# Kernel optimization log

Measured on AMD Instinct MI355X. Metric: run time of the kernel, lower is better.

The kernel has to match this reference:

```python
import jax, jax.numpy as jnp
import numpy as np

V, H, L, B = 32000, 1024, 2, 64
TEMP = 0.8


def setup_inputs() -> dict:
    key = jax.random.key(0)
    ks = jax.random.split(key, 12)
    sV = 1.0 / np.sqrt(V)
    sH = 1.0 / np.sqrt(H)
    return {
        "x": jax.random.normal(ks[0], (B, V), jnp.float32),
        "hidden_states": jax.random.normal(ks[1], (L, B, H), jnp.float32),
        "cell_states": jax.random.normal(ks[2], (L, B, H), jnp.float32),
        # gate order along axis 1: f, i, o, g
        "Wh": jax.random.uniform(ks[3], (L, 4, H, H), jnp.float32, -sH, sH),
        "bh": jax.random.uniform(ks[4], (L, 4, H), jnp.float32, -sH, sH),
        "Wx0": jax.random.uniform(ks[5], (4, H, V), jnp.float32, -sV, sV),
        "bx0": jax.random.uniform(ks[6], (4, H), jnp.float32, -sV, sV),
        "Wx1": jax.random.uniform(ks[7], (4, H, H), jnp.float32, -sH, sH),
        "bx1": jax.random.uniform(ks[8], (4, H), jnp.float32, -sH, sH),
        "Wdec": jax.random.uniform(ks[9], (V, H), jnp.float32, -sH, sH),
        "bdec": jax.random.uniform(ks[10], (V,), jnp.float32, -sH, sH),
    }


def _lstm_cell(inp, h, c, Wx, bx, Whl, bhl):
    # fused gate pre-activations: [B, 4, H]
    z = (jnp.einsum("ghk,bk->bgh", Wx, inp) + bx[None]
         + jnp.einsum("ghk,bk->bgh", Whl, h) + bhl[None])
    f = jax.nn.sigmoid(z[:, 0])
    i = jax.nn.sigmoid(z[:, 1])
    o = jax.nn.sigmoid(z[:, 2])
    g = jnp.tanh(z[:, 3])
    c_new = f * c + i * g
    out = o * jnp.tanh(c_new)
    return out, c_new


def reference(x, hidden_states, cell_states, Wh, bh, Wx0, bx0, Wx1, bx1, Wdec, bdec):
    wx = [(Wx0, bx0), (Wx1, bx1)]
    outputs, cstates = [], []
    inp = x
    for l in range(L):
        out, c_new = _lstm_cell(inp, hidden_states[l], cell_states[l],
                                wx[l][0], wx[l][1], Wh[l], bh[l])
        outputs.append(out)
        cstates.append(c_new)
        inp = out
    logits = outputs[-1] @ Wdec.T + bdec
    logp = jax.nn.log_softmax(logits / TEMP, axis=-1)
    return logp, jnp.stack(outputs), jnp.stack(cstates)
```

## Files before the change

kernel.cpp:

```cpp
#include <hip/hip_runtime.h>
#include <hip/hip_bf16.h>
#include <cstdint>

#define DI __device__ __forceinline__

typedef __attribute__((ext_vector_type(8))) short short8;
typedef __attribute__((ext_vector_type(4))) float f32x4;
typedef __attribute__((ext_vector_type(4))) int int4v;

DI f32x4 mfma16(short8 a, short8 b, f32x4 c) {
  return __builtin_amdgcn_mfma_f32_16x16x32_bf16(a, b, c, 0, 0, 0);
}

DI uint32_t f2bf(float f) {
  uint32_t u = __float_as_uint(f);
  return (u + 0x7fffu + ((u >> 16) & 1u)) >> 16;
}

DI uint32_t pk2(float a, float b) {
  return f2bf(a) | (f2bf(b) << 16);
}

DI short8 cvt8(float4 a, float4 b) {
  int4v t;
  t.x = (int)pk2(a.x, a.y);
  t.y = (int)pk2(a.z, a.w);
  t.z = (int)pk2(b.x, b.y);
  t.w = (int)pk2(b.z, b.w);
  return __builtin_bit_cast(short8, t);
}

__global__ __launch_bounds__(256, 3) void gates_f32(
    const float* __restrict__ x, const float* __restrict__ hs,
    const float* __restrict__ Wx0, const float* __restrict__ Wh,
    float* __restrict__ zpart) {
  const int y = blockIdx.y;
  const float* A;
  const float* W;
  int ldA, K, steps;
  long kbase;
  if (y < 40) {
    A = x; ldA = 32000; W = Wx0; K = 32000; steps = 25;
    kbase = (long)y * 800;
  } else if (y < 44) {
    A = hs; ldA = 1024; W = Wh; K = 1024; steps = 8;
    kbase = (long)(y - 40) * 256;
  } else {
    A = hs + 65536; ldA = 1024; W = Wh + 4194304; K = 1024; steps = 8;
    kbase = (long)(y - 44) * 256;
  }
  const int tid = threadIdx.x;
  const int wv = tid >> 6;
  const int lane = tid & 63;
  const int l15 = lane & 15;
  const int l4 = lane >> 4;
  const int h = blockIdx.x * 64 + wv * 16 + l15;

  const float* arow[4];
#pragma unroll
  for (int m = 0; m < 4; ++m)
    arow[m] = A + (size_t)(m * 16 + l15) * ldA + kbase + l4 * 8;
  const float* wrow[4];
#pragma unroll
  for (int g = 0; g < 4; ++g)
    wrow[g] = W + (size_t)(g * 1024 + h) * K + kbase + l4 * 8;

  f32x4 acc[4][4];
#pragma unroll
  for (int g = 0; g < 4; ++g)
#pragma unroll
    for (int m = 0; m < 4; ++m)
      acc[g][m] = f32x4{0.f, 0.f, 0.f, 0.f};

  for (int s = 0; s < steps; ++s) {
    short8 af[4];
#pragma unroll
    for (int m = 0; m < 4; ++m) {
      const float* ap = arow[m] + (size_t)s * 32;
      float4 a0 = *(const float4*)ap;
      float4 a1 = *(const float4*)(ap + 4);
      af[m] = cvt8(a0, a1);
    }
#pragma unroll
    for (int g = 0; g < 4; ++g) {
      const float* wp = wrow[g] + (size_t)s * 32;
      float4 w0 = *(const float4*)wp;
      float4 w1 = *(const float4*)(wp + 4);
      short8 bfr = cvt8(w0, w1);
#pragma unroll
      for (int m = 0; m < 4; ++m)
        acc[g][m] = mfma16(af[m], bfr, acc[g][m]);
    }
  }

  float* zp = zpart + (size_t)y * 262144 + (size_t)(l4 * 4) * 4096 + h;
#pragma unroll
  for (int g = 0; g < 4; ++g)
#pragma unroll
    for (int m = 0; m < 4; ++m)
#pragma unroll
      for (int r = 0; r < 4; ++r)
        zp[(size_t)(m * 16 + r) * 4096 + g * 1024] = acc[g][m][r];
}

__global__ __launch_bounds__(256) void gates_b16(
    const ushort* __restrict__ A, const float* __restrict__ W,
    float* __restrict__ zbase) {
  const int chunk = blockIdx.y;
  const long kbase = (long)chunk * 64;
  const int tid = threadIdx.x;
  const int wv = tid >> 6;
  const int lane = tid & 63;
  const int l15 = lane & 15;
  const int l4 = lane >> 4;
  const int h = blockIdx.x * 64 + wv * 16 + l15;

  const ushort* arow[4];
#pragma unroll
  for (int m = 0; m < 4; ++m)
    arow[m] = A + (size_t)(m * 16 + l15) * 1024 + kbase + l4 * 8;
  const float* wrow[4];
#pragma unroll
  for (int g = 0; g < 4; ++g)
    wrow[g] = W + (size_t)(g * 1024 + h) * 1024 + kbase + l4 * 8;

  f32x4 acc[4][4];
#pragma unroll
  for (int g = 0; g < 4; ++g)
#pragma unroll
    for (int m = 0; m < 4; ++m)
      acc[g][m] = f32x4{0.f, 0.f, 0.f, 0.f};

#pragma unroll
  for (int s = 0; s < 2; ++s) {
    short8 af[4];
#pragma unroll
    for (int m = 0; m < 4; ++m)
      af[m] = *(const short8*)(arow[m] + (size_t)s * 32);
#pragma unroll
    for (int g = 0; g < 4; ++g) {
      const float* wp = wrow[g] + (size_t)s * 32;
      float4 w0 = *(const float4*)wp;
      float4 w1 = *(const float4*)(wp + 4);
      short8 bfr = cvt8(w0, w1);
#pragma unroll
      for (int m = 0; m < 4; ++m)
        acc[g][m] = mfma16(af[m], bfr, acc[g][m]);
    }
  }

  float* zp = zbase + (size_t)chunk * 262144 + (size_t)(l4 * 4) * 4096 + h;
#pragma unroll
  for (int g = 0; g < 4; ++g)
#pragma unroll
    for (int m = 0; m < 4; ++m)
#pragma unroll
      for (int r = 0; r < 4; ++r)
        zp[(size_t)(m * 16 + r) * 4096 + g * 1024] = acc[g][m][r];
}

__global__ __launch_bounds__(256) void lstm_cell_k(
    const float* __restrict__ zpart, int nslots,
    const float* __restrict__ bx, const float* __restrict__ bhl,
    const float* __restrict__ c_in,
    float* __restrict__ h_out, float* __restrict__ c_out,
    ushort* __restrict__ h_out_b) {
  int idx = blockIdx.x * 256 + threadIdx.x;
  if (idx >= 64 * 1024) return;
  int h = idx & 1023;
  float z0 = bx[h] + bhl[h];
  float z1 = bx[1024 + h] + bhl[1024 + h];
  float z2 = bx[2048 + h] + bhl[2048 + h];
  float z3 = bx[3072 + h] + bhl[3072 + h];
  int b = idx >> 10;
  const float* zp = zpart + (size_t)b * 4096 + h;
  for (int s = 0; s < nslots; ++s) {
    const float* p = zp + (size_t)s * 262144;
    z0 += p[0];
    z1 += p[1024];
    z2 += p[2048];
    z3 += p[3072];
  }
  float f = 1.f / (1.f + expf(-z0));
  float i = 1.f / (1.f + expf(-z1));
  float o = 1.f / (1.f + expf(-z2));
  float g = tanhf(z3);
  float c = f * c_in[idx] + i * g;
  float hv = o * tanhf(c);
  h_out[idx] = hv;
  c_out[idx] = c;
  h_out_b[idx] = (ushort)f2bf(hv);
}

__global__ __launch_bounds__(64) void gemm_dec(
    const ushort* __restrict__ A, const float* __restrict__ W,
    const float* __restrict__ bias, float* __restrict__ logits) {
  const int lane = threadIdx.x;
  const int l15 = lane & 15;
  const int l4 = lane >> 4;
  const int col = blockIdx.x * 16 + l15;

  const ushort* arow[4];
#pragma unroll
  for (int m = 0; m < 4; ++m)
    arow[m] = A + (size_t)(m * 16 + l15) * 1024 + l4 * 8;
  const float* wrow = W + (size_t)col * 1024 + l4 * 8;

  f32x4 acc[4];
#pragma unroll
  for (int m = 0; m < 4; ++m) acc[m] = f32x4{0.f, 0.f, 0.f, 0.f};

  for (int s = 0; s < 32; ++s) {
    short8 af[4];
#pragma unroll
    for (int m = 0; m < 4; ++m)
      af[m] = *(const short8*)(arow[m] + (size_t)s * 32);
    const float* wp = wrow + (size_t)s * 32;
    float4 w0 = *(const float4*)wp;
    float4 w1 = *(const float4*)(wp + 4);
    short8 bfr = cvt8(w0, w1);
#pragma unroll
    for (int m = 0; m < 4; ++m)
      acc[m] = mfma16(af[m], bfr, acc[m]);
  }

  float bv = bias[col];
  float* lp = logits + (size_t)(l4 * 4) * 32000 + col;
#pragma unroll
  for (int m = 0; m < 4; ++m)
#pragma unroll
    for (int r = 0; r < 4; ++r)
      lp[(size_t)(m * 16 + r) * 32000] = acc[m][r] + bv;
}

__global__ __launch_bounds__(256) void softmax_part1(
    const float* __restrict__ logits, float2* __restrict__ ms) {
  const int cx = blockIdx.x;
  const int b = blockIdx.y;
  const int tid = threadIdx.x;
  const int wv = tid >> 6;
  const int lane = tid & 63;
  const float* row = logits + (size_t)b * 32000 + cx * 8000;
  __shared__ float rbuf[4];

  float m = -1e30f;
  for (int i = tid; i < 8000; i += 256) m = fmaxf(m, row[i]);
#pragma unroll
  for (int d = 1; d < 64; d <<= 1) m = fmaxf(m, __shfl_xor(m, d));
  if (lane == 0) rbuf[wv] = m;
  __syncthreads();
  m = fmaxf(fmaxf(rbuf[0], rbuf[1]), fmaxf(rbuf[2], rbuf[3]));
  __syncthreads();

  float sum = 0.f;
  for (int i = tid; i < 8000; i += 256) sum += expf((row[i] - m) * 1.25f);
#pragma unroll
  for (int d = 1; d < 64; d <<= 1) sum += __shfl_xor(sum, d);
  if (lane == 0) rbuf[wv] = sum;
  __syncthreads();
  if (tid == 0) {
    sum = rbuf[0] + rbuf[1] + rbuf[2] + rbuf[3];
    ms[b * 4 + cx] = make_float2(m, sum);
  }
}

__global__ __launch_bounds__(256) void softmax_part2(
    const float* __restrict__ logits, const float2* __restrict__ ms,
    float* __restrict__ logp) {
  const int cx = blockIdx.x;
  const int b = blockIdx.y;
  const int tid = threadIdx.x;

  float2 p0 = ms[b * 4 + 0], p1 = ms[b * 4 + 1];
  float2 p2 = ms[b * 4 + 2], p3 = ms[b * 4 + 3];
  float M = fmaxf(fmaxf(p0.x, p1.x), fmaxf(p2.x, p3.x));
  float S = p0.y * expf((p0.x - M) * 1.25f) + p1.y * expf((p1.x - M) * 1.25f) +
            p2.y * expf((p2.x - M) * 1.25f) + p3.y * expf((p3.x - M) * 1.25f);
  float lse = logf(S);

  const float* row = logits + (size_t)b * 32000 + cx * 4000;
  float* op = logp + (size_t)b * 32000 + cx * 4000;
  for (int i = tid; i < 4000; i += 256)
    op[i] = (row[i] - M) * 1.25f - lse;
}

extern "C" void kernel_launch(void* const* d_in, const int* in_sizes, int n_in,
                              void* d_out, int out_size, void* d_ws, size_t ws_size,
                              hipStream_t stream) {
  const float* x    = (const float*)d_in[0];
  const float* hs   = (const float*)d_in[1];
  const float* cs   = (const float*)d_in[2];
  const float* Wh   = (const float*)d_in[3];
  const float* bh   = (const float*)d_in[4];
  const float* Wx0  = (const float*)d_in[5];
  const float* bx0  = (const float*)d_in[6];
  const float* Wx1  = (const float*)d_in[7];
  const float* bx1  = (const float*)d_in[8];
  const float* Wdec = (const float*)d_in[9];
  const float* bdec = (const float*)d_in[10];

  float* out   = (float*)d_out;
  float* logp  = out;
  float* houts = out + 2048000;
  float* couts = out + 2179072;

  char* ws = (char*)d_ws;
  ushort* outb   = (ushort*)ws;
  float*  logits = (float*)(ws + 262144);
  float2* ms     = (float2*)(ws + 262144 + 8192000);
  float*  zpart  = (float*)(ws + 262144 + 8192000 + 2048);

  gates_f32<<<dim3(16, 48), 256, 0, stream>>>(x, hs, Wx0, Wh, zpart);

  lstm_cell_k<<<256, 256, 0, stream>>>(zpart, 44, bx0, bh, cs,
                                       houts, couts, outb);

  gates_b16<<<dim3(16, 16), 256, 0, stream>>>(
      outb, Wx1, zpart + (size_t)48 * 262144);

  lstm_cell_k<<<256, 256, 0, stream>>>(zpart + (size_t)44 * 262144, 20,
                                       bx1, bh + 4096, cs + 65536,
                                       houts + 65536, couts + 65536,
                                       outb + 65536);

  gemm_dec<<<2000, 64, 0, stream>>>(outb + 65536, Wdec, bdec, logits);

  softmax_part1<<<dim3(4, 64), 256, 0, stream>>>(logits, ms);
  softmax_part2<<<dim3(8, 64), 256, 0, stream>>>(logits, ms, logp);
}
```

Before: 277.2 us.

## Widen per-lane K contiguity to 128-float strips and cut split-K partial count

Each lane now loads 32 contiguous floats (eight float4s) per step instead of 8, so one row fetch covers four MFMA k-slices. The mapping of K to lanes is permuted consistently for A and W, so the dot products are unchanged. The split-K factor drops (gates_f32 48→29 slots, gates_b16 16→8), which means fewer partial sums to write and reduce in the lstm_cell kernels. The cost is higher register pressure (occupancy hint lowered from 3 to 2) and fewer blocks in flight for the big weight stream.

```diff
diff --git a/kernel.cpp b/kernel.cpp
--- a/kernel.cpp
+++ b/kernel.cpp
@@ -30,24 +30,24 @@
   return __builtin_bit_cast(short8, t);
 }
 
-__global__ __launch_bounds__(256, 3) void gates_f32(
+__global__ __launch_bounds__(256, 2) void gates_f32(
     const float* __restrict__ x, const float* __restrict__ hs,
     const float* __restrict__ Wx0, const float* __restrict__ Wh,
     float* __restrict__ zpart) {
   const int y = blockIdx.y;
   const float* A;
   const float* W;
-  int ldA, K, steps;
+  int ldA, K, nss;
   long kbase;
-  if (y < 40) {
-    A = x; ldA = 32000; W = Wx0; K = 32000; steps = 25;
-    kbase = (long)y * 800;
-  } else if (y < 44) {
-    A = hs; ldA = 1024; W = Wh; K = 1024; steps = 8;
-    kbase = (long)(y - 40) * 256;
+  if (y < 25) {
+    A = x; ldA = 32000; W = Wx0; K = 32000; nss = 10;
+    kbase = (long)y * 1280;
+  } else if (y < 27) {
+    A = hs; ldA = 1024; W = Wh; K = 1024; nss = 4;
+    kbase = (long)(y - 25) * 512;
   } else {
-    A = hs + 65536; ldA = 1024; W = Wh + 4194304; K = 1024; steps = 8;
-    kbase = (long)(y - 44) * 256;
+    A = hs + 65536; ldA = 1024; W = Wh + 4194304; K = 1024; nss = 4;
+    kbase = (long)(y - 27) * 512;
   }
   const int tid = threadIdx.x;
   const int wv = tid >> 6;
@@ -59,11 +59,11 @@
   const float* arow[4];
 #pragma unroll
   for (int m = 0; m < 4; ++m)
-    arow[m] = A + (size_t)(m * 16 + l15) * ldA + kbase + l4 * 8;
+    arow[m] = A + (size_t)(m * 16 + l15) * ldA + kbase + l4 * 32;
   const float* wrow[4];
 #pragma unroll
   for (int g = 0; g < 4; ++g)
-    wrow[g] = W + (size_t)(g * 1024 + h) * K + kbase + l4 * 8;
+    wrow[g] = W + (size_t)(g * 1024 + h) * K + kbase + l4 * 32;
 
   f32x4 acc[4][4];
 #pragma unroll
@@ -72,24 +72,30 @@
     for (int m = 0; m < 4; ++m)
       acc[g][m] = f32x4{0.f, 0.f, 0.f, 0.f};
 
-  for (int s = 0; s < steps; ++s) {
-    short8 af[4];
+  for (int ss = 0; ss < nss; ++ss) {
+    short8 af[4][4];
 #pragma unroll
     for (int m = 0; m < 4; ++m) {
-      const float* ap = arow[m] + (size_t)s * 32;
-      float4 a0 = *(const float4*)ap;
-      float4 a1 = *(const float4*)(ap + 4);
-      af[m] = cvt8(a0, a1);
+      const float* ap = arow[m] + (size_t)ss * 128;
+      float4 av[8];
+#pragma unroll
+      for (int t = 0; t < 8; ++t) av[t] = *(const float4*)(ap + t * 4);
+#pragma unroll
+      for (int j = 0; j < 4; ++j) af[m][j] = cvt8(av[2 * j], av[2 * j + 1]);
     }
 #pragma unroll
     for (int g = 0; g < 4; ++g) {
-      const float* wp = wrow[g] + (size_t)s * 32;
-      float4 w0 = *(const float4*)wp;
-      float4 w1 = *(const float4*)(wp + 4);
-      short8 bfr = cvt8(w0, w1);
-#pragma unroll
-      for (int m = 0; m < 4; ++m)
-        acc[g][m] = mfma16(af[m], bfr, acc[g][m]);
+      const float* wp = wrow[g] + (size_t)ss * 128;
+      float4 wvv[8];
+#pragma unroll
+      for (int t = 0; t < 8; ++t) wvv[t] = *(const float4*)(wp + t * 4);
+#pragma unroll
+      for (int j = 0; j < 4; ++j) {
+        short8 bfr = cvt8(wvv[2 * j], wvv[2 * j + 1]);
+#pragma unroll
+        for (int m = 0; m < 4; ++m)
+          acc[g][m] = mfma16(af[m][j], bfr, acc[g][m]);
+      }
     }
   }
 
@@ -107,7 +113,7 @@
     const ushort* __restrict__ A, const float* __restrict__ W,
     float* __restrict__ zbase) {
   const int chunk = blockIdx.y;
-  const long kbase = (long)chunk * 64;
+  const long kbase = (long)chunk * 128;
   const int tid = threadIdx.x;
   const int wv = tid >> 6;
   const int lane = tid & 63;
@@ -115,14 +121,14 @@
   const int l4 = lane >> 4;
   const int h = blockIdx.x * 64 + wv * 16 + l15;
 
-  const ushort* arow[4];
-#pragma unroll
-  for (int m = 0; m < 4; ++m)
-    arow[m] = A + (size_t)(m * 16 + l15) * 1024 + kbase + l4 * 8;
-  const float* wrow[4];
-#pragma unroll
-  for (int g = 0; g < 4; ++g)
-    wrow[g] = W + (size_t)(g * 1024 + h) * 1024 + kbase + l4 * 8;
+  short8 af[4][4];
+#pragma unroll
+  for (int m = 0; m < 4; ++m) {
+    const ushort* ap = A + (size_t)(m * 16 + l15) * 1024 + kbase + l4 * 32;
+#pragma unroll
+    for (int j = 0; j < 4; ++j)
+      af[m][j] = *(const short8*)(ap + j * 8);
+  }
 
   f32x4 acc[4][4];
 #pragma unroll
@@ -132,20 +138,17 @@
       acc[g][m] = f32x4{0.f, 0.f, 0.f, 0.f};
 
 #pragma unroll
-  for (int s = 0; s < 2; ++s) {
-    short8 af[4];
-#pragma unroll
-    for (int m = 0; m < 4; ++m)
-      af[m] = *(const short8*)(arow[m] + (size_t)s * 32);
-#pragma unroll
-    for (int g = 0; g < 4; ++g) {
-      const float* wp = wrow[g] + (size_t)s * 32;
-      float4 w0 = *(const float4*)wp;
-      float4 w1 = *(const float4*)(wp + 4);
-      short8 bfr = cvt8(w0, w1);
+  for (int g = 0; g < 4; ++g) {
+    const float* wp = W + (size_t)(g * 1024 + h) * 1024 + kbase + l4 * 32;
+    float4 wvv[8];
+#pragma unroll
+    for (int t = 0; t < 8; ++t) wvv[t] = *(const float4*)(wp + t * 4);
+#pragma unroll
+    for (int j = 0; j < 4; ++j) {
+      short8 bfr = cvt8(wvv[2 * j], wvv[2 * j + 1]);
 #pragma unroll
       for (int m = 0; m < 4; ++m)
-        acc[g][m] = mfma16(af[m], bfr, acc[g][m]);
+        acc[g][m] = mfma16(af[m][j], bfr, acc[g][m]);
     }
   }
 
@@ -203,25 +206,34 @@
   const ushort* arow[4];
 #pragma unroll
   for (int m = 0; m < 4; ++m)
-    arow[m] = A + (size_t)(m * 16 + l15) * 1024 + l4 * 8;
-  const float* wrow = W + (size_t)col * 1024 + l4 * 8;
+    arow[m] = A + (size_t)(m * 16 + l15) * 1024 + l4 * 32;
+  const float* wrow = W + (size_t)col * 1024 + l4 * 32;
 
   f32x4 acc[4];
 #pragma unroll
   for (int m = 0; m < 4; ++m) acc[m] = f32x4{0.f, 0.f, 0.f, 0.f};
 
-  for (int s = 0; s < 32; ++s) {
-    short8 af[4];
-#pragma unroll
-    for (int m = 0; m < 4; ++m)
-      af[m] = *(const short8*)(arow[m] + (size_t)s * 32);
-    const float* wp = wrow + (size_t)s * 32;
-    float4 w0 = *(const float4*)wp;
-    float4 w1 = *(const float4*)(wp + 4);
-    short8 bfr = cvt8(w0, w1);
-#pragma unroll
-    for (int m = 0; m < 4; ++m)
-      acc[m] = mfma16(af[m], bfr, acc[m]);
+#pragma unroll
+  for (int ss = 0; ss < 8; ++ss) {
+    short8 af[4][4];
+#pragma unroll
+    for (int m = 0; m < 4; ++m) {
+      const ushort* ap = arow[m] + (size_t)ss * 128;
+#pragma unroll
+      for (int j = 0; j < 4; ++j)
+        af[m][j] = *(const short8*)(ap + j * 8);
+    }
+    const float* wp = wrow + (size_t)ss * 128;
+    float4 wvv[8];
+#pragma unroll
+    for (int t = 0; t < 8; ++t) wvv[t] = *(const float4*)(wp + t * 4);
+#pragma unroll
+    for (int j = 0; j < 4; ++j) {
+      short8 bfr = cvt8(wvv[2 * j], wvv[2 * j + 1]);
+#pragma unroll
+      for (int m = 0; m < 4; ++m)
+        acc[m] = mfma16(af[m][j], bfr, acc[m]);
+    }
   }
 
   float bv = bias[col];
@@ -310,15 +322,15 @@
   float2* ms     = (float2*)(ws + 262144 + 8192000);
   float*  zpart  = (float*)(ws + 262144 + 8192000 + 2048);
 
-  gates_f32<<<dim3(16, 48), 256, 0, stream>>>(x, hs, Wx0, Wh, zpart);
-
-  lstm_cell_k<<<256, 256, 0, stream>>>(zpart, 44, bx0, bh, cs,
+  gates_f32<<<dim3(16, 29), 256, 0, stream>>>(x, hs, Wx0, Wh, zpart);
+
+  lstm_cell_k<<<256, 256, 0, stream>>>(zpart, 27, bx0, bh, cs,
                                        houts, couts, outb);
 
-  gates_b16<<<dim3(16, 16), 256, 0, stream>>>(
-      outb, Wx1, zpart + (size_t)48 * 262144);
-
-  lstm_cell_k<<<256, 256, 0, stream>>>(zpart + (size_t)44 * 262144, 20,
+  gates_b16<<<dim3(16, 8), 256, 0, stream>>>(
+      outb, Wx1, zpart + (size_t)29 * 262144);
+
+  lstm_cell_k<<<256, 256, 0, stream>>>(zpart + (size_t)27 * 262144, 10,
                                        bx1, bh + 4096, cs + 65536,
                                        houts + 65536, couts + 65536,
                                        outb + 65536);
```

Measured after the change: 510.8 us. +84.3%, slower.

## Pre-convert activations to bf16 and software-pipeline weight loads in gate GEMM

Applied to the files above, without the earlier changes.

Adds a separate kernel that converts x and the hidden states to bf16 once, so the gate GEMM reads half-width activations and no longer converts them inside every block. The gate GEMM now handles 64 K per step with two MFMAs and prefetches the next step's fp32 weights into registers while the current MFMAs run. The K split is coarser (29 partial slices instead of 48), which shrinks the partial-sum buffer the cell kernel has to reduce. The cost is an extra launch and a round trip of the bf16 copy of x through memory, plus higher register pressure that lowers the occupancy hint from 3 to 2.

```diff
diff --git a/kernel.cpp b/kernel.cpp
--- a/kernel.cpp
+++ b/kernel.cpp
@@ -30,24 +30,46 @@
   return __builtin_bit_cast(short8, t);
 }
 
-__global__ __launch_bounds__(256, 3) void gates_f32(
+__global__ __launch_bounds__(256) void convert_k(
     const float* __restrict__ x, const float* __restrict__ hs,
+    ushort* __restrict__ xb, ushort* __restrict__ hb) {
+  const int NX4 = 512000;
+  const int NH4 = 32768;
+  int i = blockIdx.x * 256 + threadIdx.x;
+  if (i < NX4) {
+    float4 v = *(const float4*)(x + 4 * (size_t)i);
+    uint2 o;
+    o.x = pk2(v.x, v.y);
+    o.y = pk2(v.z, v.w);
+    *(uint2*)(xb + 4 * (size_t)i) = o;
+  } else if (i < NX4 + NH4) {
+    int j = i - NX4;
+    float4 v = *(const float4*)(hs + 4 * (size_t)j);
+    uint2 o;
+    o.x = pk2(v.x, v.y);
+    o.y = pk2(v.z, v.w);
+    *(uint2*)(hb + 4 * (size_t)j) = o;
+  }
+}
+
+__global__ __launch_bounds__(256, 2) void gates_pf(
+    const ushort* __restrict__ xb, const ushort* __restrict__ hb,
     const float* __restrict__ Wx0, const float* __restrict__ Wh,
     float* __restrict__ zpart) {
   const int y = blockIdx.y;
-  const float* A;
+  const ushort* A;
   const float* W;
   int ldA, K, steps;
   long kbase;
-  if (y < 40) {
-    A = x; ldA = 32000; W = Wx0; K = 32000; steps = 25;
-    kbase = (long)y * 800;
-  } else if (y < 44) {
-    A = hs; ldA = 1024; W = Wh; K = 1024; steps = 8;
-    kbase = (long)(y - 40) * 256;
+  if (y < 25) {
+    A = xb; ldA = 32000; W = Wx0; K = 32000; steps = 20;
+    kbase = (long)y * 1280;
+  } else if (y < 27) {
+    A = hb; ldA = 1024; W = Wh; K = 1024; steps = 8;
+    kbase = (long)(y - 25) * 512;
   } else {
-    A = hs + 65536; ldA = 1024; W = Wh + 4194304; K = 1024; steps = 8;
-    kbase = (long)(y - 44) * 256;
+    A = hb + 65536; ldA = 1024; W = Wh + 4194304; K = 1024; steps = 8;
+    kbase = (long)(y - 27) * 512;
   }
   const int tid = threadIdx.x;
   const int wv = tid >> 6;
@@ -56,7 +78,7 @@
   const int l4 = lane >> 4;
   const int h = blockIdx.x * 64 + wv * 16 + l15;
 
-  const float* arow[4];
+  const ushort* arow[4];
 #pragma unroll
   for (int m = 0; m < 4; ++m)
     arow[m] = A + (size_t)(m * 16 + l15) * ldA + kbase + l4 * 8;
@@ -72,24 +94,54 @@
     for (int m = 0; m < 4; ++m)
       acc[g][m] = f32x4{0.f, 0.f, 0.f, 0.f};
 
+  float4 wt[4][4];
+  short8 wb0[4], wb1[4];
+
+#pragma unroll
+  for (int g = 0; g < 4; ++g) {
+    const float* wp = wrow[g];
+    wt[g][0] = *(const float4*)wp;
+    wt[g][1] = *(const float4*)(wp + 4);
+    wt[g][2] = *(const float4*)(wp + 32);
+    wt[g][3] = *(const float4*)(wp + 36);
+  }
+#pragma unroll
+  for (int g = 0; g < 4; ++g) {
+    wb0[g] = cvt8(wt[g][0], wt[g][1]);
+    wb1[g] = cvt8(wt[g][2], wt[g][3]);
+  }
+
   for (int s = 0; s < steps; ++s) {
-    short8 af[4];
+    short8 af0[4], af1[4];
 #pragma unroll
     for (int m = 0; m < 4; ++m) {
-      const float* ap = arow[m] + (size_t)s * 32;
-      float4 a0 = *(const float4*)ap;
-      float4 a1 = *(const float4*)(ap + 4);
-      af[m] = cvt8(a0, a1);
+      const ushort* ap = arow[m] + (size_t)s * 64;
+      af0[m] = *(const short8*)ap;
+      af1[m] = *(const short8*)(ap + 32);
     }
-#pragma unroll
-    for (int g = 0; g < 4; ++g) {
-      const float* wp = wrow[g] + (size_t)s * 32;
-      float4 w0 = *(const float4*)wp;
-      float4 w1 = *(const float4*)(wp + 4);
-      short8 bfr = cvt8(w0, w1);
-#pragma unroll
-      for (int m = 0; m < 4; ++m)
-        acc[g][m] = mfma16(af[m], bfr, acc[g][m]);
+    if (s + 1 < steps) {
+#pragma unroll
+      for (int g = 0; g < 4; ++g) {
+        const float* wp = wrow[g] + (size_t)(s + 1) * 64;
+        wt[g][0] = *(const float4*)wp;
+        wt[g][1] = *(const float4*)(wp + 4);
+        wt[g][2] = *(const float4*)(wp + 32);
+        wt[g][3] = *(const float4*)(wp + 36);
+      }
+    }
+#pragma unroll
+    for (int g = 0; g < 4; ++g)
+#pragma unroll
+      for (int m = 0; m < 4; ++m) {
+        acc[g][m] = mfma16(af0[m], wb0[g], acc[g][m]);
+        acc[g][m] = mfma16(af1[m], wb1[g], acc[g][m]);
+      }
+    if (s + 1 < steps) {
+#pragma unroll
+      for (int g = 0; g < 4; ++g) {
+        wb0[g] = cvt8(wt[g][0], wt[g][1]);
+        wb1[g] = cvt8(wt[g][2], wt[g][3]);
+      }
     }
   }
 
@@ -305,20 +357,24 @@
   float* couts = out + 2179072;
 
   char* ws = (char*)d_ws;
-  ushort* outb   = (ushort*)ws;
-  float*  logits = (float*)(ws + 262144);
-  float2* ms     = (float2*)(ws + 262144 + 8192000);
-  float*  zpart  = (float*)(ws + 262144 + 8192000 + 2048);
-
-  gates_f32<<<dim3(16, 48), 256, 0, stream>>>(x, hs, Wx0, Wh, zpart);
-
-  lstm_cell_k<<<256, 256, 0, stream>>>(zpart, 44, bx0, bh, cs,
+  ushort* xb     = (ushort*)ws;
+  ushort* hb     = (ushort*)(ws + 4096000);
+  ushort* outb   = (ushort*)(ws + 4358144);
+  float*  logits = (float*)(ws + 4620288);
+  float2* ms     = (float2*)(ws + 12812288);
+  float*  zpart  = (float*)(ws + 12814336);
+
+  convert_k<<<2128, 256, 0, stream>>>(x, hs, xb, hb);
+
+  gates_pf<<<dim3(16, 29), 256, 0, stream>>>(xb, hb, Wx0, Wh, zpart);
+
+  lstm_cell_k<<<256, 256, 0, stream>>>(zpart, 27, bx0, bh, cs,
                                        houts, couts, outb);
 
   gates_b16<<<dim3(16, 16), 256, 0, stream>>>(
-      outb, Wx1, zpart + (size_t)48 * 262144);
-
-  lstm_cell_k<<<256, 256, 0, stream>>>(zpart + (size_t)44 * 262144, 20,
+      outb, Wx1, zpart + (size_t)29 * 262144);
+
+  lstm_cell_k<<<256, 256, 0, stream>>>(zpart + (size_t)27 * 262144, 18,
                                        bx1, bh + 4096, cs + 65536,
                                        houts + 65536, couts + 65536,
                                        outb + 65536);
```

After: 280.6 us. About the same (+1.2%).
